# Kernel optimization log

Hardware: AMD Instinct MI355X
Metric: run time of the kernel (lower is better)

The kernel has to match this reference:

```python
import jax, jax.numpy as jnp
import numpy as np
from jax import lax

_SQ2 = np.sqrt(2.0)
_H2 = (np.array([[1.0, 1.0], [1.0, -1.0]]) / _SQ2).astype(np.complex64)
_BN_INV = 1.0 / np.sqrt(1.0 + 1e-5)  # eval-mode BN, running_mean=0, running_var=1

# wire 0 is the most-significant bit of the 4-qubit basis index (PennyLane convention)
def _cnot_perm(c, t):
    p = np.arange(16)
    for b in range(16):
        if (b >> (3 - c)) & 1:
            p[b] = b ^ (1 << (3 - t))
    return p

# CNOT(0,1) then CNOT(1,2) then CNOT(2,3) then CNOT(3,0); psi_out = psi_in[perm]
_p01, _p12, _p23, _p30 = _cnot_perm(0, 1), _cnot_perm(1, 2), _cnot_perm(2, 3), _cnot_perm(3, 0)
_PTOT = _p01[_p12[_p23[_p30]]]
# PauliZ expectation signs: (16 basis states, 4 wires)
_ZM = np.array([[1.0 - 2.0 * ((b >> (3 - w)) & 1) for w in range(4)] for b in range(16)], np.float32)


def _make_unitaries(w0, w1):
    """w0, w1: (C,2). Circuit: H^4 -> RY(w0[0],w0[1],w0[0],w0[1]) -> RZ(w1 same pattern) -> CNOT ring."""
    ty = jnp.stack([w0[:, 0], w0[:, 1], w0[:, 0], w0[:, 1]], axis=1)  # (C,4)
    tz = jnp.stack([w1[:, 0], w1[:, 1], w1[:, 0], w1[:, 1]], axis=1)
    c, s = jnp.cos(ty / 2), jnp.sin(ty / 2)
    ry = jnp.stack([jnp.stack([c, -s], -1), jnp.stack([s, c], -1)], -2).astype(jnp.complex64)  # (C,4,2,2)
    ph = jnp.exp(-0.5j * tz.astype(jnp.complex64))  # (C,4)
    zr = jnp.zeros_like(ph)
    rz = jnp.stack([jnp.stack([ph, zr], -1), jnp.stack([zr, jnp.conj(ph)], -1)], -2)  # (C,4,2,2)
    g = rz @ ry @ jnp.asarray(_H2)  # per-wire single-qubit gate, (C,4,2,2)
    U = g[:, 0]
    for w in range(1, 4):  # kron over wires 0..3
        d = U.shape[1]
        U = jnp.einsum('cij,ckl->cikjl', U, g[:, w]).reshape(U.shape[0], d * 2, d * 2)
    return U[:, _PTOT, :]  # fold the CNOT-ring permutation into U


def _conv_bn_relu(x, w, g, b):
    y = lax.conv_general_dilated(x, w, (1, 1), ((1, 1), (1, 1)),
                                 dimension_numbers=('NCHW', 'OIHW', 'NCHW'))
    y = y * (g * _BN_INV)[None, :, None, None] + b[None, :, None, None]
    return jax.nn.relu(y)


def _bn_relu(x, g, b):
    return jax.nn.relu(x * (g * _BN_INV)[None, :, None, None] + b[None, :, None, None])


def _maxpool2(x):
    return lax.reduce_window(x, -jnp.inf, lax.max, (1, 1, 2, 2), (1, 1, 2, 2), 'VALID')


def _quantum_stage(e4, q_w0, q_w1):
    B, C, H, W = e4.shape
    xp = jnp.pad(e4, ((0, 0), (0, 0), (1, 2), (1, 2)))  # F.pad(1,2,1,2)
    # 4x4 patches, stride 1, row-major (matches torch unfold->view ordering): (B,C,H,W,16)
    patches = jnp.stack([xp[:, :, i:i + H, j:j + W] for i in range(4) for j in range(4)], axis=-1)
    nrm = jnp.sqrt(jnp.sum(patches * patches, axis=-1, keepdims=True))
    psi0 = (patches / jnp.maximum(nrm, 1e-12)).astype(jnp.complex64)  # AmplitudeEmbedding(normalize=True)
    U = _make_unitaries(q_w0, q_w1)  # (C,16,16) complex
    psi = jnp.einsum('cij,bchwj->bchwi', U, psi0)
    probs = psi.real ** 2 + psi.imag ** 2
    ev = jnp.einsum('bchwi,iq->bchwq', probs, jnp.asarray(_ZM))  # <Z_w> per wire
    return (ev.mean(-1) + 1.0) / 2.0


def setup_inputs() -> dict:
    key = jax.random.key(0)
    ks = jax.random.split(key, 18)
    conv_w = lambda k, o, i: jax.random.normal(k, (o, i, 3, 3), jnp.float32) / np.sqrt(i * 9)
    gamma = lambda k, c: jax.random.uniform(k, (c,), jnp.float32, 0.75, 1.25)
    beta = lambda k, c: 0.1 * jax.random.normal(k, (c,), jnp.float32)
    return {
        'x': jax.random.normal(ks[0], (8, 1, 256, 256), jnp.float32),
        'w1': conv_w(ks[1], 32, 1), 'g1': gamma(ks[2], 32), 'b1': beta(ks[3], 32),
        'w2': conv_w(ks[4], 64, 32), 'g2': gamma(ks[5], 64), 'b2': beta(ks[6], 64),
        'w3': conv_w(ks[7], 128, 64), 'g3': gamma(ks[8], 128), 'b3': beta(ks[9], 128),
        'w4': conv_w(ks[10], 256, 128), 'g4': gamma(ks[11], 256), 'b4': beta(ks[12], 256),
        'q_w0': 0.5 * jax.random.normal(ks[13], (256, 2), jnp.float32),
        'q_w1': 0.5 * jax.random.normal(ks[14], (256, 2), jnp.float32),
        'g5': gamma(ks[15], 256), 'b5': beta(ks[16], 256),
    }


def reference(x, w1, g1, b1, w2, g2, b2, w3, g3, b3, w4, g4, b4, q_w0, q_w1, g5, b5):
    e1 = _conv_bn_relu(x, w1, g1, b1)                 # (8,32,256,256)
    e2 = _conv_bn_relu(_maxpool2(e1), w2, g2, b2)     # (8,64,128,128)
    e3 = _conv_bn_relu(_maxpool2(e2), w3, g3, b3)     # (8,128,64,64)
    e4 = _conv_bn_relu(_maxpool2(e3), w4, g4, b4)     # (8,256,32,32)
    q = _quantum_stage(e4, q_w0, q_w1)                # (8,256,32,32)
    out4 = _bn_relu(q, g5, b5)
    return (e1, e2, e3, out4)
```

## Files before the change

### kernel.cpp

```cpp
#include <hip/hip_runtime.h>
#include <cstdint>
#include <cstddef>

#define BN_INV 0.9999950000374997f

typedef __attribute__((ext_vector_type(8))) _Float16 h8v;
typedef __attribute__((ext_vector_type(4))) float f4v;

__device__ __forceinline__ void fsplit(float v, ushort& h, ushort& l) {
    _Float16 hh = (_Float16)v;
    _Float16 ll = (_Float16)(v - (float)hh);
    h = __builtin_bit_cast(ushort, hh);
    l = __builtin_bit_cast(ushort, ll);
}

__device__ __forceinline__ void repack_one(
    const float* __restrict__ w, ushort* __restrict__ dst, int CIN, int i)
{
    int ocf = i / (CIN * 9);
    int r = i % (CIN * 9);
    int ic = r / 9;
    int tap = r % 9;
    int ocg = ocf >> 6, oc = ocf & 63;
    int chunk = ic >> 5, q = (ic >> 3) & 3, j = ic & 7;
    int nch = CIN >> 5;
    ushort h, l;
    fsplit(w[i], h, l);
    size_t base = (size_t)((ocg * nch + chunk) * 2) * 18432
                + (size_t)tap * 2048 + q * 512 + oc * 8 + j;
    dst[base] = h;
    dst[base + 18432] = l;
}

__global__ __launch_bounds__(256) void prep_conv1_kernel(
    const float* __restrict__ w0, const float* __restrict__ w1,
    float* __restrict__ U,
    const float* __restrict__ w2, ushort* __restrict__ wb2,
    const float* __restrict__ w3, ushort* __restrict__ wb3,
    const float* __restrict__ w4, ushort* __restrict__ wb4,
    const float* __restrict__ x, const float* __restrict__ wt,
    const float* __restrict__ g, const float* __restrict__ be,
    float* __restrict__ out, ushort* __restrict__ pooled)
{
    __shared__ float s_in[10][34];
    __shared__ float s_w[384];

    int blk = blockIdx.x;
    int tid = threadIdx.x;

    if (blk >= 2048) {
        if (blk >= 2424)     { repack_one(w4, wb4, 128, (blk - 2424) * 256 + tid); return; }
        if (blk >= 2136)     { repack_one(w3, wb3,  64, (blk - 2136) * 256 + tid); return; }
        if (blk >= 2064)     { repack_one(w2, wb2,  32, (blk - 2064) * 256 + tid); return; }

        int idx = (blk - 2048) * 256 + tid;
        int c = idx >> 4, r = idx & 15;
        float gr[4][2][2], gi[4][2][2];
        const float inv_sq2 = 0.70710678118654752f;
#pragma unroll
        for (int w = 0; w < 4; ++w) {
            float ty = w0[c * 2 + (w & 1)];
            float tz = w1[c * 2 + (w & 1)];
            float cy = cosf(0.5f * ty), sy = sinf(0.5f * ty);
            float cz = cosf(0.5f * tz), sz = sinf(0.5f * tz);
            float r00 = (cy - sy) * inv_sq2, r01 = (cy + sy) * inv_sq2;
            float r10 = (cy + sy) * inv_sq2, r11 = (sy - cy) * inv_sq2;
            gr[w][0][0] = cz * r00; gi[w][0][0] = -sz * r00;
            gr[w][0][1] = cz * r01; gi[w][0][1] = -sz * r01;
            gr[w][1][0] = cz * r10; gi[w][1][0] =  sz * r10;
            gr[w][1][1] = cz * r11; gi[w][1][1] =  sz * r11;
        }
        const int PTOT[16] = {0,13,3,14,6,11,5,8,12,1,15,2,10,7,9,4};
        int rp = PTOT[r];
        float* Uo = U + (size_t)c * 512 + r * 32;
#pragma unroll
        for (int cc = 0; cc < 16; ++cc) {
            float pr = 1.f, pi = 0.f;
#pragma unroll
            for (int w = 0; w < 4; ++w) {
                int ib = (rp >> (3 - w)) & 1, jb = (cc >> (3 - w)) & 1;
                float ar = gr[w][ib][jb], ai = gi[w][ib][jb];
                float nr = pr * ar - pi * ai;
                float ni = pr * ai + pi * ar;
                pr = nr; pi = ni;
            }
            Uo[cc * 2 + 0] = pr;
            Uo[cc * 2 + 1] = pi;
        }
        return;
    }

    int bid = blk;
    int tile = bid & 255;
    int b = bid >> 8;
    int tx0 = (tile & 7) * 32, ty0 = (tile >> 3) * 8;

    for (int i = tid; i < 288; i += 256) s_w[(i / 9) * 12 + (i % 9)] = wt[i];
    for (int i = tid; i < 340; i += 256) {
        int yy = i / 34, xx = i % 34;
        int gy = ty0 + yy - 1, gx = tx0 + xx - 1;
        float v = 0.f;
        if (gy >= 0 && gy < 256 && gx >= 0 && gx < 256)
            v = x[(size_t)b * 65536 + gy * 256 + gx];
        s_in[yy][xx] = v;
    }
    __syncthreads();

    int px = tid & 31, py = tid >> 5;
    float t[3][3];
#pragma unroll
    for (int i = 0; i < 3; ++i)
#pragma unroll
        for (int j = 0; j < 3; ++j) t[i][j] = s_in[py + i][px + j];

    bool wr_pool = ((px & 1) == 0) && ((py & 1) == 0);
    ushort* op = pooled + (((size_t)b * 128 + ((ty0 + py) >> 1)) * 128 + ((tx0 + px) >> 1)) * 64;

    size_t obase = ((size_t)b * 32) * 65536 + (size_t)(ty0 + py) * 256 + (tx0 + px);
#pragma unroll
    for (int k = 0; k < 4; ++k) {
        uint4 uh, ul;
#pragma unroll
        for (int j = 0; j < 8; ++j) {
            const int oc = k * 8 + j;
            const float4 wa = *(const float4*)&s_w[oc * 12];
            const float4 wc = *(const float4*)&s_w[oc * 12 + 4];
            const float w8 = s_w[oc * 12 + 8];
            float s = wa.x * t[0][0] + wa.y * t[0][1] + wa.z * t[0][2]
                    + wa.w * t[1][0] + wc.x * t[1][1] + wc.y * t[1][2]
                    + wc.z * t[2][0] + wc.w * t[2][1] + w8  * t[2][2];
            s = s * (g[oc] * BN_INV) + be[oc];
            s = fmaxf(s, 0.f);
            out[obase + (size_t)oc * 65536] = s;
            float p = fmaxf(s, __shfl_xor(s, 1));
            p = fmaxf(p, __shfl_xor(p, 32));
            ushort h, l;
            fsplit(p, h, l);
            uint hw = (uint)h, lw = (uint)l;
            if (j == 0) { uh.x = hw; ul.x = lw; }
            else if (j == 1) { uh.x |= hw << 16; ul.x |= lw << 16; }
            else if (j == 2) { uh.y = hw; ul.y = lw; }
            else if (j == 3) { uh.y |= hw << 16; ul.y |= lw << 16; }
            else if (j == 4) { uh.z = hw; ul.z = lw; }
            else if (j == 5) { uh.z |= hw << 16; ul.z |= lw << 16; }
            else if (j == 6) { uh.w = hw; ul.w = lw; }
            else             { uh.w |= hw << 16; ul.w |= lw << 16; }
        }
        if (wr_pool) {
            *(uint4*)(op + 8 * k) = uh;
            *(uint4*)(op + 32 + 8 * k) = ul;
        }
    }
}

template <int CIN, int COUT, int HW, bool POOL>
__global__ __launch_bounds__(512) void conv3x3_mfma_split(
    const ushort* __restrict__ in,
    const ushort* __restrict__ wb,
    const float* __restrict__ g, const float* __restrict__ be,
    float* __restrict__ out,
    ushort* __restrict__ pooled)
{
    constexpr int NCH = CIN / 32;
    constexpr int NTX = HW / 16;
    constexpr int NT = NTX * (HW / 8);
    constexpr int NOCG = COUT / 64;
    constexpr int PS = 72;
    constexpr int BUFSZ = 180 * PS;
    constexpr int NBUF = (NCH > 1) ? 2 : 1;

    __shared__ __align__(16) ushort s_in[NBUF * BUFSZ];

    constexpr int NWG = NT * NOCG * 8;
    int bid = blockIdx.x;
    bid = (bid & 7) * (NWG >> 3) + (bid >> 3);

    int tile = bid % NT;
    int rest = bid / NT;
    int ocg = rest % NOCG;
    int b = rest / NOCG;
    int x0 = (tile % NTX) * 16;
    int y0 = (tile / NTX) * 8;

    int tid = threadIdx.x;
    int wv = tid >> 6;
    int lane = tid & 63;
    int n = lane & 15;
    int q = lane >> 4;
    int oc_half = (wv & 1) * 32;
    int sg = wv >> 1;

    int ib[2];
#pragma unroll
    for (int f = 0; f < 2; ++f)
        ib[f] = ((sg * 2 + f) * 18 + n) * PS + q * 8;
    int iwa0 = q * 512 + (oc_half + n) * 8;
    int iwa1 = q * 512 + (oc_half + 16 + n) * 8;

    const ushort* inb = in + (size_t)b * HW * HW * 2 * CIN;

    f4v acc[2][2];
#pragma unroll
    for (int a = 0; a < 2; ++a)
#pragma unroll
        for (int f = 0; f < 2; ++f) acc[a][f] = (f4v){0.f, 0.f, 0.f, 0.f};

    auto stage = [&](int ch, int bsel) {
#pragma unroll
        for (int it = 0; it < 6; ++it) {
            int i = tid + it * 512;
            if (i < 2880) {
                int pos = i >> 4;
                int r2 = i & 15;
                int comp = r2 >> 3;
                int u = r2 & 7;
                int py = pos / 18, px = pos % 18;
                int gy = y0 - 1 + py, gx = x0 - 1 + px;
                uint2 v; v.x = 0u; v.y = 0u;
                if (gy >= 0 && gy < HW && gx >= 0 && gx < HW)
                    v = *(const uint2*)(inb + ((size_t)gy * HW + gx) * (2 * CIN)
                                        + comp * CIN + ch * 32 + u * 4);
                *(uint2*)(&s_in[bsel * BUFSZ + pos * PS + comp * 32 + u * 4]) = v;
            }
        }
    };

    stage(0, 0);
    int cur = 0;
    for (int ch = 0; ch < NCH; ++ch) {
        __syncthreads();
        if (ch + 1 < NCH) stage(ch + 1, cur ^ 1);

        const ushort* wc = wb + (size_t)((ocg * NCH + ch) * 2) * 18432;
        const ushort* sb = &s_in[cur * BUFSZ];
        __builtin_amdgcn_s_setprio(1);
#pragma unroll 3
        for (int tap = 0; tap < 9; ++tap) {
            const int toff = ((tap / 3) * 18 + (tap % 3)) * PS;
            const ushort* wt_ = wc + tap * 2048;
            h8v ah0 = *(const h8v*)(wt_ + iwa0);
            h8v ah1 = *(const h8v*)(wt_ + iwa1);
            h8v al0 = *(const h8v*)(wt_ + 18432 + iwa0);
            h8v al1 = *(const h8v*)(wt_ + 18432 + iwa1);
            h8v bh[2], bl[2];
#pragma unroll
            for (int f = 0; f < 2; ++f) {
                bh[f] = *(const h8v*)(&sb[toff + ib[f]]);
                bl[f] = *(const h8v*)(&sb[toff + ib[f] + 32]);
            }
#pragma unroll
            for (int f = 0; f < 2; ++f) {
                acc[0][f] = __builtin_amdgcn_mfma_f32_16x16x32_f16(ah0, bh[f], acc[0][f], 0, 0, 0);
                acc[1][f] = __builtin_amdgcn_mfma_f32_16x16x32_f16(ah1, bh[f], acc[1][f], 0, 0, 0);
            }
#pragma unroll
            for (int f = 0; f < 2; ++f) {
                acc[0][f] = __builtin_amdgcn_mfma_f32_16x16x32_f16(ah0, bl[f], acc[0][f], 0, 0, 0);
                acc[1][f] = __builtin_amdgcn_mfma_f32_16x16x32_f16(ah1, bl[f], acc[1][f], 0, 0, 0);
            }
#pragma unroll
            for (int f = 0; f < 2; ++f) {
                acc[0][f] = __builtin_amdgcn_mfma_f32_16x16x32_f16(al0, bh[f], acc[0][f], 0, 0, 0);
                acc[1][f] = __builtin_amdgcn_mfma_f32_16x16x32_f16(al1, bh[f], acc[1][f], 0, 0, 0);
            }
        }
        __builtin_amdgcn_s_setprio(0);
        cur ^= (NBUF - 1);
    }

    float vr[2][2][4];
#pragma unroll
    for (int tf = 0; tf < 2; ++tf)
#pragma unroll
        for (int f = 0; f < 2; ++f) {
            int y = y0 + sg * 2 + f;
#pragma unroll
            for (int r = 0; r < 4; ++r) {
                int oc = ocg * 64 + oc_half + tf * 16 + q * 4 + r;
                float v = fmaxf(acc[tf][f][r] * (g[oc] * BN_INV) + be[oc], 0.f);
                vr[tf][f][r] = v;
                out[((size_t)(b * COUT + oc) * HW + y) * HW + (x0 + n)] = v;
            }
        }

    if (POOL) {
#pragma unroll
        for (int tf = 0; tf < 2; ++tf) {
            ushort h[4], l[4];
#pragma unroll
            for (int r = 0; r < 4; ++r) {
                float p = fmaxf(vr[tf][0][r], vr[tf][1][r]);
                p = fmaxf(p, __shfl_xor(p, 1));
                fsplit(p, h[r], l[r]);
            }
            if ((n & 1) == 0) {
                int pyp = (y0 >> 1) + sg;
                int pxp = (x0 + n) >> 1;
                int ocb = ocg * 64 + oc_half + tf * 16 + q * 4;
                ushort* op = pooled
                    + (((size_t)b * (HW / 2) + pyp) * (HW / 2) + pxp) * (2 * COUT);
                uint2 uh, ul;
                uh.x = (uint)h[0] | ((uint)h[1] << 16);
                uh.y = (uint)h[2] | ((uint)h[3] << 16);
                ul.x = (uint)l[0] | ((uint)l[1] << 16);
                ul.y = (uint)l[2] | ((uint)l[3] << 16);
                *(uint2*)(op + ocb) = uh;
                *(uint2*)(op + COUT + ocb) = ul;
            }
        }
    }
}

__global__ __launch_bounds__(256) void quantum_bn_relu(
    const float* __restrict__ e4,
    const float* __restrict__ U,
    const float* __restrict__ g5, const float* __restrict__ b5,
    float* __restrict__ out)
{
    int blk = blockIdx.x;
    int c = blk & 255;
    __shared__ float sp[35][35];
    __shared__ __align__(16) float sU[512];

    int tid = threadIdx.x;
    for (int i = tid; i < 1225; i += 256) ((float*)sp)[i] = 0.f;
    const float4* Usrc = (const float4*)(U + (size_t)c * 512);
    if (tid < 128) ((float4*)sU)[tid] = Usrc[tid];
    float4 pv = ((const float4*)(e4 + (size_t)blk * 1024))[tid];
    __syncthreads();
    {
        int y = tid >> 3, x4 = (tid & 7) << 2;
        sp[y + 1][x4 + 1] = pv.x;
        sp[y + 1][x4 + 2] = pv.y;
        sp[y + 1][x4 + 3] = pv.z;
        sp[y + 1][x4 + 4] = pv.w;
    }
    __syncthreads();

    float t[4][16];
    float inv2[4];
#pragma unroll
    for (int k = 0; k < 4; ++k) {
        int site = tid + 256 * k;
        int y = site >> 5, x = site & 31;
        float ss = 0.f;
#pragma unroll
        for (int i = 0; i < 4; ++i)
#pragma unroll
            for (int j = 0; j < 4; ++j) {
                float v = sp[y + i][x + j];
                t[k][i * 4 + j] = v;
                ss += v * v;
            }
        float inv = 1.f / fmaxf(sqrtf(ss), 1e-12f);
        inv2[k] = inv * inv;
    }

    const int   RI[10] = {0, 1, 2, 4, 7, 8, 11, 13, 14, 15};
    const float ZM[10] = {1.f, .5f, .5f, .5f, -.5f, .5f, -.5f, -.5f, -.5f, -1.f};
    const float4* sU4 = (const float4*)sU;

    float s[4] = {0.f, 0.f, 0.f, 0.f};
#pragma unroll
    for (int ii = 0; ii < 10; ++ii) {
        int i = RI[ii];
        float re[4] = {0.f, 0.f, 0.f, 0.f};
        float im[4] = {0.f, 0.f, 0.f, 0.f};
#pragma unroll
        for (int jj = 0; jj < 8; ++jj) {
            float4 u = sU4[i * 8 + jj];
#pragma unroll
            for (int k = 0; k < 4; ++k) {
                re[k] += u.x * t[k][2 * jj];
                im[k] += u.y * t[k][2 * jj];
                re[k] += u.z * t[k][2 * jj + 1];
                im[k] += u.w * t[k][2 * jj + 1];
            }
        }
        float zm = ZM[ii];
#pragma unroll
        for (int k = 0; k < 4; ++k)
            s[k] += (re[k] * re[k] + im[k] * im[k]) * zm;
    }

    float sc = g5[c] * BN_INV, bi = b5[c];
#pragma unroll
    for (int k = 0; k < 4; ++k) {
        float q = (s[k] * inv2[k] + 1.f) * 0.5f;
        float o = fmaxf(q * sc + bi, 0.f);
        out[(size_t)blk * 1024 + tid + 256 * k] = o;
    }
}

extern "C" void kernel_launch(void* const* d_in, const int* in_sizes, int n_in,
                              void* d_out, int out_size, void* d_ws, size_t ws_size,
                              hipStream_t stream)
{
    const float* x   = (const float*)d_in[0];
    const float* w1  = (const float*)d_in[1];
    const float* g1  = (const float*)d_in[2];
    const float* b1  = (const float*)d_in[3];
    const float* w2  = (const float*)d_in[4];
    const float* g2  = (const float*)d_in[5];
    const float* b2  = (const float*)d_in[6];
    const float* w3  = (const float*)d_in[7];
    const float* g3  = (const float*)d_in[8];
    const float* b3  = (const float*)d_in[9];
    const float* w4  = (const float*)d_in[10];
    const float* g4  = (const float*)d_in[11];
    const float* b4  = (const float*)d_in[12];
    const float* qw0 = (const float*)d_in[13];
    const float* qw1 = (const float*)d_in[14];
    const float* g5  = (const float*)d_in[15];
    const float* b5  = (const float*)d_in[16];

    float* out = (float*)d_out;
    float* e1  = out;
    float* e2  = out + 16777216;
    float* e3  = out + 25165824;
    float* o4  = out + 29360128;

    float* ws = (float*)d_ws;
    float*  Uw  = ws;
    ushort* wb2 = (ushort*)(ws + 131072);
    ushort* wb3 = (ushort*)(ws + 149504);
    ushort* wb4 = (ushort*)(ws + 223232);
    ushort* pt1 = (ushort*)(ws + 518144);
    ushort* pt2 = (ushort*)(ws + 4712448);
    ushort* pt3 = (ushort*)(ws + 518144);

    prep_conv1_kernel<<<2048 + 1528, 256, 0, stream>>>(
        qw0, qw1, Uw, w2, wb2, w3, wb3, w4, wb4,
        x, w1, g1, b1, e1, pt1);

    conv3x3_mfma_split<32, 64, 128, true><<<1024, 512, 0, stream>>>(pt1, wb2, g2, b2, e2, pt2);

    conv3x3_mfma_split<64, 128, 64, true><<<512, 512, 0, stream>>>(pt2, wb3, g3, b3, e3, pt3);

    conv3x3_mfma_split<128, 256, 32, false><<<256, 512, 0, stream>>>(pt3, wb4, g4, b4, o4, nullptr);

    quantum_bn_relu<<<2048, 256, 0, stream>>>(o4, Uw, g5, b5, o4);
}
```

Before: 246.8 us.

## Retile conv1 into pool-quad thread groups and vectorize the quantum stage's window loads

After: 248.2 us. Within noise of the previous version (+0.6%).

```diff
diff --git a/kernel.cpp b/kernel.cpp
--- a/kernel.cpp
+++ b/kernel.cpp
@@ -6,6 +6,7 @@
 
 typedef __attribute__((ext_vector_type(8))) _Float16 h8v;
 typedef __attribute__((ext_vector_type(4))) float f4v;
+typedef __attribute__((ext_vector_type(2))) float f2v;
 
 __device__ __forceinline__ void fsplit(float v, ushort& h, ushort& l) {
     _Float16 hh = (_Float16)v;
@@ -42,8 +43,7 @@
     const float* __restrict__ g, const float* __restrict__ be,
     float* __restrict__ out, ushort* __restrict__ pooled)
 {
-    __shared__ float s_in[10][34];
-    __shared__ float s_w[384];
+    __shared__ float s_in[4][132];
 
     int blk = blockIdx.x;
     int tid = threadIdx.x;
@@ -90,14 +90,13 @@
         return;
     }
 
-    int bid = blk;
-    int tile = bid & 255;
-    int b = bid >> 8;
-    int tx0 = (tile & 7) * 32, ty0 = (tile >> 3) * 8;
-
-    for (int i = tid; i < 288; i += 256) s_w[(i / 9) * 12 + (i % 9)] = wt[i];
-    for (int i = tid; i < 340; i += 256) {
-        int yy = i / 34, xx = i % 34;
+    int b = blk >> 8;
+    int rest = blk & 255;
+    int ty0 = (rest >> 1) * 2;
+    int tx0 = (rest & 1) * 128;
+
+    for (int i = tid; i < 520; i += 256) {
+        int yy = i / 130, xx = i % 130;
         int gy = ty0 + yy - 1, gx = tx0 + xx - 1;
         float v = 0.f;
         if (gy >= 0 && gy < 256 && gx >= 0 && gx < 256)
@@ -106,34 +105,32 @@
     }
     __syncthreads();
 
-    int px = tid & 31, py = tid >> 5;
+    int xx = ((tid >> 2) << 1) | (tid & 1);
+    int yy = (tid >> 1) & 1;
     float t[3][3];
 #pragma unroll
     for (int i = 0; i < 3; ++i)
 #pragma unroll
-        for (int j = 0; j < 3; ++j) t[i][j] = s_in[py + i][px + j];
-
-    bool wr_pool = ((px & 1) == 0) && ((py & 1) == 0);
-    ushort* op = pooled + (((size_t)b * 128 + ((ty0 + py) >> 1)) * 128 + ((tx0 + px) >> 1)) * 64;
-
-    size_t obase = ((size_t)b * 32) * 65536 + (size_t)(ty0 + py) * 256 + (tx0 + px);
+        for (int j = 0; j < 3; ++j) t[i][j] = s_in[yy + i][xx + j];
+
+    bool wr_pool = (tid & 3) == 0;
+    ushort* op = pooled + (((size_t)b * 128 + (ty0 >> 1)) * 128 + (tx0 >> 1) + (tid >> 2)) * 64;
+
+    size_t obase = ((size_t)b * 32) * 65536 + (size_t)(ty0 + yy) * 256 + (tx0 + xx);
 #pragma unroll
     for (int k = 0; k < 4; ++k) {
         uint4 uh, ul;
 #pragma unroll
         for (int j = 0; j < 8; ++j) {
             const int oc = k * 8 + j;
-            const float4 wa = *(const float4*)&s_w[oc * 12];
-            const float4 wc = *(const float4*)&s_w[oc * 12 + 4];
-            const float w8 = s_w[oc * 12 + 8];
-            float s = wa.x * t[0][0] + wa.y * t[0][1] + wa.z * t[0][2]
-                    + wa.w * t[1][0] + wc.x * t[1][1] + wc.y * t[1][2]
-                    + wc.z * t[2][0] + wc.w * t[2][1] + w8  * t[2][2];
+            float s = wt[oc*9+0] * t[0][0] + wt[oc*9+1] * t[0][1] + wt[oc*9+2] * t[0][2]
+                    + wt[oc*9+3] * t[1][0] + wt[oc*9+4] * t[1][1] + wt[oc*9+5] * t[1][2]
+                    + wt[oc*9+6] * t[2][0] + wt[oc*9+7] * t[2][1] + wt[oc*9+8] * t[2][2];
             s = s * (g[oc] * BN_INV) + be[oc];
             s = fmaxf(s, 0.f);
             out[obase + (size_t)oc * 65536] = s;
             float p = fmaxf(s, __shfl_xor(s, 1));
-            p = fmaxf(p, __shfl_xor(p, 32));
+            p = fmaxf(p, __shfl_xor(p, 2));
             ushort h, l;
             fsplit(p, h, l);
             uint hw = (uint)h, lw = (uint)l;
@@ -319,11 +316,11 @@
 {
     int blk = blockIdx.x;
     int c = blk & 255;
-    __shared__ float sp[35][35];
+    __shared__ float sp[35][36];
     __shared__ __align__(16) float sU[512];
 
     int tid = threadIdx.x;
-    for (int i = tid; i < 1225; i += 256) ((float*)sp)[i] = 0.f;
+    for (int i = tid; i < 35 * 36; i += 256) ((float*)sp)[i] = 0.f;
     const float4* Usrc = (const float4*)(U + (size_t)c * 512);
     if (tid < 128) ((float4*)sU)[tid] = Usrc[tid];
     float4 pv = ((const float4*)(e4 + (size_t)blk * 1024))[tid];
@@ -337,19 +334,25 @@
     }
     __syncthreads();
 
-    float t[4][16];
+    int y = tid >> 3, x4 = (tid & 7) << 2;
+    float rows[4][8];
+#pragma unroll
+    for (int i = 0; i < 4; ++i) {
+        float4 a = *(const float4*)&sp[y + i][x4];
+        float4 bq = *(const float4*)&sp[y + i][x4 + 4];
+        rows[i][0] = a.x;  rows[i][1] = a.y;  rows[i][2] = a.z;  rows[i][3] = a.w;
+        rows[i][4] = bq.x; rows[i][5] = bq.y; rows[i][6] = bq.z; rows[i][7] = bq.w;
+    }
+
     float inv2[4];
 #pragma unroll
     for (int k = 0; k < 4; ++k) {
-        int site = tid + 256 * k;
-        int y = site >> 5, x = site & 31;
         float ss = 0.f;
 #pragma unroll
         for (int i = 0; i < 4; ++i)
 #pragma unroll
             for (int j = 0; j < 4; ++j) {
-                float v = sp[y + i][x + j];
-                t[k][i * 4 + j] = v;
+                float v = rows[i][k + j];
                 ss += v * v;
             }
         float inv = 1.f / fmaxf(sqrtf(ss), 1e-12f);
@@ -364,32 +367,36 @@
 #pragma unroll
     for (int ii = 0; ii < 10; ++ii) {
         int i = RI[ii];
-        float re[4] = {0.f, 0.f, 0.f, 0.f};
-        float im[4] = {0.f, 0.f, 0.f, 0.f};
+        f2v p0 = {0.f, 0.f}, p1 = {0.f, 0.f}, p2 = {0.f, 0.f}, p3 = {0.f, 0.f};
 #pragma unroll
         for (int jj = 0; jj < 8; ++jj) {
             float4 u = sU4[i * 8 + jj];
-#pragma unroll
-            for (int k = 0; k < 4; ++k) {
-                re[k] += u.x * t[k][2 * jj];
-                im[k] += u.y * t[k][2 * jj];
-                re[k] += u.z * t[k][2 * jj + 1];
-                im[k] += u.w * t[k][2 * jj + 1];
-            }
+            f2v u01 = {u.x, u.y};
+            f2v u23 = {u.z, u.w};
+            const int e0 = 2 * jj, e1 = 2 * jj + 1;
+            p0 += u01 * rows[e0 >> 2][0 + (e0 & 3)];
+            p1 += u01 * rows[e0 >> 2][1 + (e0 & 3)];
+            p2 += u01 * rows[e0 >> 2][2 + (e0 & 3)];
+            p3 += u01 * rows[e0 >> 2][3 + (e0 & 3)];
+            p0 += u23 * rows[e1 >> 2][0 + (e1 & 3)];
+            p1 += u23 * rows[e1 >> 2][1 + (e1 & 3)];
+            p2 += u23 * rows[e1 >> 2][2 + (e1 & 3)];
+            p3 += u23 * rows[e1 >> 2][3 + (e1 & 3)];
         }
         float zm = ZM[ii];
-#pragma unroll
-        for (int k = 0; k < 4; ++k)
-            s[k] += (re[k] * re[k] + im[k] * im[k]) * zm;
+        s[0] += (p0.x * p0.x + p0.y * p0.y) * zm;
+        s[1] += (p1.x * p1.x + p1.y * p1.y) * zm;
+        s[2] += (p2.x * p2.x + p2.y * p2.y) * zm;
+        s[3] += (p3.x * p3.x + p3.y * p3.y) * zm;
     }
 
     float sc = g5[c] * BN_INV, bi = b5[c];
-#pragma unroll
-    for (int k = 0; k < 4; ++k) {
-        float q = (s[k] * inv2[k] + 1.f) * 0.5f;
-        float o = fmaxf(q * sc + bi, 0.f);
-        out[(size_t)blk * 1024 + tid + 256 * k] = o;
-    }
+    float4 o;
+    o.x = fmaxf(((s[0] * inv2[0] + 1.f) * 0.5f) * sc + bi, 0.f);
+    o.y = fmaxf(((s[1] * inv2[1] + 1.f) * 0.5f) * sc + bi, 0.f);
+    o.z = fmaxf(((s[2] * inv2[2] + 1.f) * 0.5f) * sc + bi, 0.f);
+    o.w = fmaxf(((s[3] * inv2[3] + 1.f) * 0.5f) * sc + bi, 0.f);
+    *(float4*)(out + (size_t)blk * 1024 + y * 32 + x4) = o;
 }
 
 extern "C" void kernel_launch(void* const* d_in, const int* in_sizes, int n_in,
```
